# Kernel tuning notes

Hardware: AMD Instinct MI355X
Metric: run time of the kernel (lower is better)

The kernel has to match this reference:

```python
import jax, jax.numpy as jnp
import numpy as np

N_NODES = 50000
EMBED_DIM = 512
N_EDGES = 150000


def _edge_scores(node_embeddings, edges):
    # edges: [2, E] int; dot product of endpoint embeddings -> [E]
    src = node_embeddings[edges[0]]  # [E, D]
    dst = node_embeddings[edges[1]]  # [E, D]
    return jnp.sum(src * dst, axis=1)


def setup_inputs() -> dict:
    key = jax.random.key(0)
    k1, k2, k3 = jax.random.split(key, 3)
    node_embeddings = jax.random.normal(k1, (N_NODES, EMBED_DIM), dtype=jnp.float32)
    edge_index = jax.random.randint(k2, (2, N_EDGES), 0, N_NODES, dtype=jnp.int64)
    # negative edges: uniform random node pairs (matches the original sampler's
    # fallback distribution; precomputed so the reference is deterministic/jittable)
    neg_edges = jax.random.randint(k3, (2, N_EDGES), 0, N_NODES, dtype=jnp.int64)
    return {
        "node_embeddings": node_embeddings,
        "edge_index": edge_index,
        "neg_edges": neg_edges,
        "num_nodes": N_NODES,
    }


def reference(node_embeddings, edge_index, neg_edges, num_nodes):
    pos_scores = _edge_scores(node_embeddings, edge_index)  # [E]
    neg_scores = _edge_scores(node_embeddings, neg_edges)   # [E]
    all_scores = jnp.concatenate([pos_scores, neg_scores])
    all_labels = jnp.concatenate([
        jnp.ones_like(pos_scores),
        jnp.zeros_like(neg_scores),
    ])
    # BCE with logits: log(1 + exp(s)) - s*y, numerically stable via logaddexp
    per_elem = jnp.logaddexp(jnp.float32(0.0), all_scores) - all_scores * all_labels
    return jnp.mean(per_elem)
```

## Files before the change

### kernel.cpp

```cpp
#include <hip/hip_runtime.h>
#include <math.h>

#define N_EDGES   150000
#define TOTAL     300000
#define EMBED_DIM 512
#define N_NODES   50000
#define TABLE_ELEMS (N_NODES * EMBED_DIM)
#define TABLE_BYTES_F8 ((size_t)TABLE_ELEMS)
#define BLOCK_THREADS 256
#define CONV_BLOCKS 2048

#define GROUPS16   (TOTAL / 16)
#define POS_G16    (N_EDGES / 16)

#define NCHUNK       8
#define CHUNK_BYTES  64
#define SLICE_BYTES  ((size_t)N_NODES * CHUNK_BYTES)
#define PARTIAL_BYTES ((size_t)NCHUNK * TOTAL * 4)
#define WS_ACC_OFF   (TABLE_BYTES_F8 + PARTIAL_BYTES)
#define WS_NEEDED    (WS_ACC_OFF + 64)

#define SCORE_BLOCKS 2048
#define BLOCKS_PER_CHUNK (SCORE_BLOCKS / NCHUNK)
#define WAVES_PER_CHUNK  (BLOCKS_PER_CHUNK * 4)
#define RED_BLOCKS ((TOTAL + BLOCK_THREADS - 1) / BLOCK_THREADS)

typedef float floatx4 __attribute__((ext_vector_type(4)));
typedef unsigned long long ull;
typedef ull ull2 __attribute__((ext_vector_type(2)));

__global__ __launch_bounds__(BLOCK_THREADS) void convert_fp8_chunked(
    const float4* __restrict__ in,
    int*          __restrict__ out,
    float*        __restrict__ acc,
    unsigned int* __restrict__ cnt)
{
    if (blockIdx.x == 0 && threadIdx.x == 0) { *acc = 0.0f; *cnt = 0u; }
    const int stride = gridDim.x * blockDim.x;
    for (int i = blockIdx.x * blockDim.x + threadIdx.x;
         i < TABLE_ELEMS / 4; i += stride) {
        float4 v = in[i];
        int r = 0;
        r = __builtin_amdgcn_cvt_pk_fp8_f32(v.x, v.y, r, false);
        r = __builtin_amdgcn_cvt_pk_fp8_f32(v.z, v.w, r, true);
        const int node  = i >> 7;
        const int dim4  = i & 127;
        const int chunk = dim4 >> 4;
        const int w4    = dim4 & 15;
        out[(size_t)chunk * (N_NODES * 16) + (size_t)node * 16 + w4] = r;
    }
}

__global__ __launch_bounds__(BLOCK_THREADS, 8) void edge_score_chunked(
    const unsigned char* __restrict__ emb8,
    const int*           __restrict__ pos_edges,
    const int*           __restrict__ neg_edges,
    float*               __restrict__ partial)
{
    const int wave  = threadIdx.x >> 6;
    const int lane  = threadIdx.x & 63;
    const int chunk = blockIdx.x & 7;
    const int w     = (blockIdx.x >> 3) * 4 + wave;

    const int i    = lane & 15;
    const int quad = lane >> 4;
    const bool is_diag = ((i >> 2) == quad);
    const int  dreg    = i & 3;

    const unsigned char* __restrict__ slice = emb8 + (size_t)chunk * SLICE_BYTES;
    float* __restrict__ pout = partial + (size_t)chunk * TOTAL;

    for (int g = w; g < GROUPS16; g += WAVES_PER_CHUNK) {
        const bool is_pos = (g < POS_G16);
        const int* __restrict__ edges = is_pos ? pos_edges : neg_edges;
        const int  e0a = 16 * g - (is_pos ? 0 : N_EDGES);

        const int sidx = __builtin_nontemporal_load(edges + e0a + i);
        const int tidx = __builtin_nontemporal_load(edges + N_EDGES + e0a + i);

        const ull2 a = *(const ull2*)(slice + (size_t)(unsigned)sidx * CHUNK_BYTES + quad * 16);
        const ull2 b = *(const ull2*)(slice + (size_t)(unsigned)tidx * CHUNK_BYTES + quad * 16);

        floatx4 C = {0, 0, 0, 0};
        C = __builtin_amdgcn_mfma_f32_16x16x32_fp8_fp8((long)a[0], (long)b[0], C, 0, 0, 0);
        C = __builtin_amdgcn_mfma_f32_16x16x32_fp8_fp8((long)a[1], (long)b[1], C, 0, 0, 0);

        const float s = (dreg == 0) ? C[0] : (dreg == 1) ? C[1] : (dreg == 2) ? C[2] : C[3];
        if (is_diag)
            __builtin_nontemporal_store(s, pout + 16 * g + i);
    }
}

__global__ __launch_bounds__(BLOCK_THREADS) void reduce_bce_finalize(
    const float*  __restrict__ partial,
    float*        __restrict__ acc,
    unsigned int* __restrict__ cnt,
    float*        __restrict__ out)
{
    const int e = blockIdx.x * BLOCK_THREADS + threadIdx.x;
    float term = 0.0f;
    if (e < TOTAL) {
        float s = 0.0f;
        #pragma unroll
        for (int c = 0; c < NCHUNK; c++)
            s += partial[(size_t)c * TOTAL + e];
        const float sp = fmaxf(s, 0.0f) + log1pf(expf(-fabsf(s)));
        term = sp - (e < N_EDGES ? s : 0.0f);
    }
    #pragma unroll
    for (int off = 32; off > 0; off >>= 1)
        term += __shfl_down(term, off, 64);
    __shared__ float ls[4];
    if ((threadIdx.x & 63) == 0) ls[threadIdx.x >> 6] = term;
    __syncthreads();
    if (threadIdx.x == 0) {
        atomicAdd(acc, ls[0] + ls[1] + ls[2] + ls[3]);
        __threadfence();
        const unsigned prev = atomicAdd(cnt, 1u);
        if (prev == (unsigned)(gridDim.x - 1)) {
            __threadfence();
            const float tot = atomicAdd(acc, 0.0f);
            out[0] = tot * (1.0f / (float)TOTAL);
        }
    }
}

__global__ __launch_bounds__(BLOCK_THREADS) void convert_fp8(
    const float4* __restrict__ in,
    int*          __restrict__ out,
    float*        __restrict__ acc)
{
    if (blockIdx.x == 0 && threadIdx.x == 0) *acc = 0.0f;
    const int stride = gridDim.x * blockDim.x;
    for (int i = blockIdx.x * blockDim.x + threadIdx.x;
         i < TABLE_ELEMS / 4; i += stride) {
        float4 v = in[i];
        int r = 0;
        r = __builtin_amdgcn_cvt_pk_fp8_f32(v.x, v.y, r, false);
        r = __builtin_amdgcn_cvt_pk_fp8_f32(v.z, v.w, r, true);
        out[i] = r;
    }
}

#define EDGE_BLOCKS ((GROUPS16 + 3) / 4)
__global__ __launch_bounds__(BLOCK_THREADS, 4) void edge_loss_fp8(
    const unsigned char* __restrict__ emb8,
    const int*           __restrict__ pos_edges,
    const int*           __restrict__ neg_edges,
    float*               __restrict__ acc)
{
    const int wave = threadIdx.x >> 6;
    const int lane = threadIdx.x & 63;
    const int g    = blockIdx.x * 4 + wave;
    const int i    = lane & 15;
    const int quad = lane >> 4;
    const bool is_diag = ((i >> 2) == quad);
    const int  dreg    = i & 3;
    float contrib = 0.0f;
    if (g < GROUPS16) {
        const bool is_pos = (g < POS_G16);
        const int* __restrict__ edges = is_pos ? pos_edges : neg_edges;
        const int  e0 = 16 * g - (is_pos ? 0 : N_EDGES);
        const int sidx = edges[e0 + i];
        const int tidx = edges[N_EDGES + e0 + i];
        const ull2* rA = (const ull2*)(emb8 + (size_t)sidx * EMBED_DIM + quad * 16);
        const ull2* rB = (const ull2*)(emb8 + (size_t)tidx * EMBED_DIM + quad * 16);
        ull2 a[8], b[8];
        #pragma unroll
        for (int c = 0; c < 8; c++) { a[c] = rA[c * 4]; b[c] = rB[c * 4]; }
#if __has_builtin(__builtin_amdgcn_sched_barrier)
        __builtin_amdgcn_sched_barrier(0);
#endif
        floatx4 C0 = {0,0,0,0}, C1 = {0,0,0,0}, C2 = {0,0,0,0}, C3 = {0,0,0,0};
        #pragma unroll
        for (int c = 0; c < 2; c++) {
            #pragma unroll
            for (int h = 0; h < 2; h++) {
                C0 = __builtin_amdgcn_mfma_f32_16x16x32_fp8_fp8((long)a[c][h],     (long)b[c][h],     C0, 0, 0, 0);
                C1 = __builtin_amdgcn_mfma_f32_16x16x32_fp8_fp8((long)a[2 + c][h], (long)b[2 + c][h], C1, 0, 0, 0);
                C2 = __builtin_amdgcn_mfma_f32_16x16x32_fp8_fp8((long)a[4 + c][h], (long)b[4 + c][h], C2, 0, 0, 0);
                C3 = __builtin_amdgcn_mfma_f32_16x16x32_fp8_fp8((long)a[6 + c][h], (long)b[6 + c][h], C3, 0, 0, 0);
            }
        }
        floatx4 C = (C0 + C1) + (C2 + C3);
        float s = (dreg == 0) ? C[0] : (dreg == 1) ? C[1] : (dreg == 2) ? C[2] : C[3];
        float sp = fmaxf(s, 0.0f) + log1pf(expf(-fabsf(s)));
        contrib = is_diag ? (sp - (is_pos ? s : 0.0f)) : 0.0f;
    }
    #pragma unroll
    for (int off = 32; off > 0; off >>= 1)
        contrib += __shfl_down(contrib, off, 64);
    __shared__ float ls[4];
    if (lane == 0) ls[wave] = contrib;
    __syncthreads();
    if (threadIdx.x == 0)
        atomicAdd(acc, ls[0] + ls[1] + ls[2] + ls[3]);
}

#define N_PAIRS   (TOTAL / 2)
#define POS_PAIRS (N_EDGES / 2)
#define FB_WAVES  (CONV_BLOCKS * 4)
__global__ __launch_bounds__(BLOCK_THREADS, 8) void edge_loss_f32(
    const float* __restrict__ emb,
    const int*   __restrict__ pos_edges,
    const int*   __restrict__ neg_edges,
    float*       __restrict__ acc)
{
    const int wave  = threadIdx.x >> 6;
    const int lane  = threadIdx.x & 63;
    const int gwave = blockIdx.x * 4 + wave;
    float lsum = 0.0f;
    for (int g = gwave; g < N_PAIRS; g += FB_WAVES) {
        const bool is_pos = (g < POS_PAIRS);
        const int* __restrict__ edges = is_pos ? pos_edges : neg_edges;
        const int  e0 = 2 * g - (is_pos ? 0 : N_EDGES);
        const int s0 = edges[e0],     t0 = edges[N_EDGES + e0];
        const int s1 = edges[e0 + 1], t1 = edges[N_EDGES + e0 + 1];
        const float4* rS0 = (const float4*)(emb + (size_t)s0 * EMBED_DIM) + lane;
        const float4* rT0 = (const float4*)(emb + (size_t)t0 * EMBED_DIM) + lane;
        const float4* rS1 = (const float4*)(emb + (size_t)s1 * EMBED_DIM) + lane;
        const float4* rT1 = (const float4*)(emb + (size_t)t1 * EMBED_DIM) + lane;
        float4 a0 = rS0[0], a1 = rS0[64];
        float4 b0 = rT0[0], b1 = rT0[64];
        float4 c0 = rS1[0], c1 = rS1[64];
        float4 d0 = rT1[0], d1 = rT1[64];
        float p0 = fmaf(a0.x, b0.x, fmaf(a0.y, b0.y, fmaf(a0.z, b0.z, a0.w * b0.w)));
        float p1 = fmaf(a1.x, b1.x, fmaf(a1.y, b1.y, fmaf(a1.z, b1.z, a1.w * b1.w)));
        float q0 = fmaf(c0.x, d0.x, fmaf(c0.y, d0.y, fmaf(c0.z, d0.z, c0.w * d0.w)));
        float q1 = fmaf(c1.x, d1.x, fmaf(c1.y, d1.y, fmaf(c1.z, d1.z, c1.w * d1.w)));
        float p = p0 + p1, q = q0 + q1;
        #pragma unroll
        for (int off = 32; off > 0; off >>= 1) {
            p += __shfl_down(p, off, 64);
            q += __shfl_down(q, off, 64);
        }
        const float sp_p = fmaxf(p, 0.0f) + log1pf(expf(-fabsf(p)));
        const float sp_q = fmaxf(q, 0.0f) + log1pf(expf(-fabsf(q)));
        lsum += (lane == 0) ? (sp_p + sp_q - (is_pos ? (p + q) : 0.0f)) : 0.0f;
    }
    __shared__ float ls[4];
    if (lane == 0) ls[wave] = lsum;
    __syncthreads();
    if (threadIdx.x == 0)
        atomicAdd(acc, ls[0] + ls[1] + ls[2] + ls[3]);
}

__global__ void finalize_kernel(const float* __restrict__ acc, float* __restrict__ out)
{
    if (threadIdx.x == 0)
        out[0] = acc[0] * (1.0f / (float)TOTAL);
}

extern "C" void kernel_launch(void* const* d_in, const int* in_sizes, int n_in,
                              void* d_out, int out_size, void* d_ws, size_t ws_size,
                              hipStream_t stream) {
    const float* emb = (const float*)d_in[0];
    const int*   pos = (const int*)d_in[1];
    const int*   neg = (const int*)d_in[2];
    float* out = (float*)d_out;

    if (ws_size >= WS_NEEDED) {
        unsigned char* emb8    = (unsigned char*)d_ws;
        float*         partial = (float*)((char*)d_ws + TABLE_BYTES_F8);
        float*         acc     = (float*)((char*)d_ws + WS_ACC_OFF);
        unsigned int*  cnt     = (unsigned int*)((char*)d_ws + WS_ACC_OFF + 4);
        convert_fp8_chunked<<<CONV_BLOCKS, BLOCK_THREADS, 0, stream>>>(
            (const float4*)emb, (int*)d_ws, acc, cnt);
        edge_score_chunked<<<SCORE_BLOCKS, BLOCK_THREADS, 0, stream>>>(
            emb8, pos, neg, partial);
        reduce_bce_finalize<<<RED_BLOCKS, BLOCK_THREADS, 0, stream>>>(
            partial, acc, cnt, out);
    } else if (ws_size >= TABLE_BYTES_F8 + 64) {
        unsigned char* emb8 = (unsigned char*)d_ws;
        float*         acc  = (float*)((char*)d_ws + TABLE_BYTES_F8);
        convert_fp8<<<CONV_BLOCKS, BLOCK_THREADS, 0, stream>>>(
            (const float4*)emb, (int*)d_ws, acc);
        edge_loss_fp8<<<EDGE_BLOCKS, BLOCK_THREADS, 0, stream>>>(emb8, pos, neg, acc);
        finalize_kernel<<<1, 64, 0, stream>>>(acc, out);
    } else {
        float* acc = (float*)d_ws;
        (void)hipMemsetAsync(acc, 0, sizeof(float), stream);
        edge_loss_f32<<<CONV_BLOCKS, BLOCK_THREADS, 0, stream>>>(emb, pos, neg, acc);
        finalize_kernel<<<1, 64, 0, stream>>>(acc, out);
    }
}
```

Measured before the change: 243.7 us.

## Bind embedding chunks to XCC IDs with atomic span work-stealing

The score kernel now reads the hardware XCC ID and uses it to pick which 64-byte embedding chunk slice to process. Each slice (3.2 MB) should then stay resident in that XCD's L2 rather than relying on the block-to-XCD mapping. Work is handed out dynamically through a per-chunk atomic counter in spans of 24 groups, and each wave processes two groups per iteration for more memory-level parallelism. The convert kernel is reordered so its writes are contiguous and its reads strided, and it zeroes the claim counters. A risk is that an unbalanced number of blocks per XCC leaves chunks processed unevenly, and the atomic-plus-syncthreads loop adds overhead.

```diff
diff --git a/kernel.cpp b/kernel.cpp
--- a/kernel.cpp
+++ b/kernel.cpp
@@ -21,8 +21,9 @@
 #define WS_NEEDED    (WS_ACC_OFF + 64)
 
 #define SCORE_BLOCKS 2048
-#define BLOCKS_PER_CHUNK (SCORE_BLOCKS / NCHUNK)
-#define WAVES_PER_CHUNK  (BLOCKS_PER_CHUNK * 4)
+#define SPAN_GROUPS  24
+#define G_PER_WAVE   6
+#define NSPANS       ((GROUPS16 + SPAN_GROUPS - 1) / SPAN_GROUPS)
 #define RED_BLOCKS ((TOTAL + BLOCK_THREADS - 1) / BLOCK_THREADS)
 
 typedef float floatx4 __attribute__((ext_vector_type(4)));
@@ -33,21 +34,25 @@
     const float4* __restrict__ in,
     int*          __restrict__ out,
     float*        __restrict__ acc,
-    unsigned int* __restrict__ cnt)
-{
-    if (blockIdx.x == 0 && threadIdx.x == 0) { *acc = 0.0f; *cnt = 0u; }
+    unsigned int* __restrict__ cnt,
+    int*          __restrict__ claim)
+{
+    if (blockIdx.x == 0 && threadIdx.x < 16) {
+        if (threadIdx.x == 0) { *acc = 0.0f; *cnt = 0u; }
+        if (threadIdx.x < NCHUNK) claim[threadIdx.x] = 0;
+    }
     const int stride = gridDim.x * blockDim.x;
-    for (int i = blockIdx.x * blockDim.x + threadIdx.x;
-         i < TABLE_ELEMS / 4; i += stride) {
-        float4 v = in[i];
+    for (int o = blockIdx.x * blockDim.x + threadIdx.x;
+         o < TABLE_ELEMS / 4; o += stride) {
+        const int chunk = o / (N_NODES * 16);
+        const int rem   = o - chunk * (N_NODES * 16);
+        const int node  = rem >> 4;
+        const int w4    = rem & 15;
+        float4 v = in[node * 128 + chunk * 16 + w4];
         int r = 0;
         r = __builtin_amdgcn_cvt_pk_fp8_f32(v.x, v.y, r, false);
         r = __builtin_amdgcn_cvt_pk_fp8_f32(v.z, v.w, r, true);
-        const int node  = i >> 7;
-        const int dim4  = i & 127;
-        const int chunk = dim4 >> 4;
-        const int w4    = dim4 & 15;
-        out[(size_t)chunk * (N_NODES * 16) + (size_t)node * 16 + w4] = r;
+        out[o] = r;
     }
 }
 
@@ -55,13 +60,15 @@
     const unsigned char* __restrict__ emb8,
     const int*           __restrict__ pos_edges,
     const int*           __restrict__ neg_edges,
-    float*               __restrict__ partial)
-{
-    const int wave  = threadIdx.x >> 6;
-    const int lane  = threadIdx.x & 63;
-    const int chunk = blockIdx.x & 7;
-    const int w     = (blockIdx.x >> 3) * 4 + wave;
-
+    float*               __restrict__ partial,
+    int*                 __restrict__ claim)
+{
+    unsigned int xcc;
+    asm volatile("s_getreg_b32 %0, hwreg(HW_REG_XCC_ID)" : "=s"(xcc));
+    const int chunk = (int)(xcc & 7u);
+
+    const int wave = threadIdx.x >> 6;
+    const int lane = threadIdx.x & 63;
     const int i    = lane & 15;
     const int quad = lane >> 4;
     const bool is_diag = ((i >> 2) == quad);
@@ -70,24 +77,51 @@
     const unsigned char* __restrict__ slice = emb8 + (size_t)chunk * SLICE_BYTES;
     float* __restrict__ pout = partial + (size_t)chunk * TOTAL;
 
-    for (int g = w; g < GROUPS16; g += WAVES_PER_CHUNK) {
-        const bool is_pos = (g < POS_G16);
-        const int* __restrict__ edges = is_pos ? pos_edges : neg_edges;
-        const int  e0a = 16 * g - (is_pos ? 0 : N_EDGES);
-
-        const int sidx = __builtin_nontemporal_load(edges + e0a + i);
-        const int tidx = __builtin_nontemporal_load(edges + N_EDGES + e0a + i);
-
-        const ull2 a = *(const ull2*)(slice + (size_t)(unsigned)sidx * CHUNK_BYTES + quad * 16);
-        const ull2 b = *(const ull2*)(slice + (size_t)(unsigned)tidx * CHUNK_BYTES + quad * 16);
-
-        floatx4 C = {0, 0, 0, 0};
-        C = __builtin_amdgcn_mfma_f32_16x16x32_fp8_fp8((long)a[0], (long)b[0], C, 0, 0, 0);
-        C = __builtin_amdgcn_mfma_f32_16x16x32_fp8_fp8((long)a[1], (long)b[1], C, 0, 0, 0);
-
-        const float s = (dreg == 0) ? C[0] : (dreg == 1) ? C[1] : (dreg == 2) ? C[2] : C[3];
-        if (is_diag)
-            __builtin_nontemporal_store(s, pout + 16 * g + i);
+    __shared__ int sspan;
+    for (;;) {
+        if (threadIdx.x == 0) sspan = atomicAdd(claim + chunk, 1);
+        __syncthreads();
+        const int span = sspan;
+        __syncthreads();
+        if (span >= NSPANS) break;
+
+        const int gb = span * SPAN_GROUPS + wave * G_PER_WAVE;
+        #pragma unroll
+        for (int u = 0; u < G_PER_WAVE / 2; u++) {
+            int g0 = gb + 2 * u;
+            if (g0 > GROUPS16 - 1) g0 = GROUPS16 - 1;
+            int g1 = g0 + 1;
+            if (g1 > GROUPS16 - 1) g1 = GROUPS16 - 1;
+
+            const bool p0 = (g0 < POS_G16), p1 = (g1 < POS_G16);
+            const int* __restrict__ ed0 = p0 ? pos_edges : neg_edges;
+            const int* __restrict__ ed1 = p1 ? pos_edges : neg_edges;
+            const int e00 = 16 * g0 - (p0 ? 0 : N_EDGES);
+            const int e01 = 16 * g1 - (p1 ? 0 : N_EDGES);
+
+            const int s0 = __builtin_nontemporal_load(ed0 + e00 + i);
+            const int t0 = __builtin_nontemporal_load(ed0 + N_EDGES + e00 + i);
+            const int s1 = __builtin_nontemporal_load(ed1 + e01 + i);
+            const int t1 = __builtin_nontemporal_load(ed1 + N_EDGES + e01 + i);
+
+            const ull2 a0 = *(const ull2*)(slice + (size_t)(unsigned)s0 * CHUNK_BYTES + quad * 16);
+            const ull2 b0 = *(const ull2*)(slice + (size_t)(unsigned)t0 * CHUNK_BYTES + quad * 16);
+            const ull2 a1 = *(const ull2*)(slice + (size_t)(unsigned)s1 * CHUNK_BYTES + quad * 16);
+            const ull2 b1 = *(const ull2*)(slice + (size_t)(unsigned)t1 * CHUNK_BYTES + quad * 16);
+
+            floatx4 C0 = {0, 0, 0, 0}, C1 = {0, 0, 0, 0};
+            C0 = __builtin_amdgcn_mfma_f32_16x16x32_fp8_fp8((long)a0[0], (long)b0[0], C0, 0, 0, 0);
+            C0 = __builtin_amdgcn_mfma_f32_16x16x32_fp8_fp8((long)a0[1], (long)b0[1], C0, 0, 0, 0);
+            C1 = __builtin_amdgcn_mfma_f32_16x16x32_fp8_fp8((long)a1[0], (long)b1[0], C1, 0, 0, 0);
+            C1 = __builtin_amdgcn_mfma_f32_16x16x32_fp8_fp8((long)a1[1], (long)b1[1], C1, 0, 0, 0);
+
+            const float sc0 = (dreg == 0) ? C0[0] : (dreg == 1) ? C0[1] : (dreg == 2) ? C0[2] : C0[3];
+            const float sc1 = (dreg == 0) ? C1[0] : (dreg == 1) ? C1[1] : (dreg == 2) ? C1[2] : C1[3];
+            if (is_diag) {
+                __builtin_nontemporal_store(sc0, pout + 16 * g0 + i);
+                __builtin_nontemporal_store(sc1, pout + 16 * g1 + i);
+            }
+        }
     }
 }
 
@@ -264,10 +298,11 @@
         float*         partial = (float*)((char*)d_ws + TABLE_BYTES_F8);
         float*         acc     = (float*)((char*)d_ws + WS_ACC_OFF);
         unsigned int*  cnt     = (unsigned int*)((char*)d_ws + WS_ACC_OFF + 4);
+        int*           claim   = (int*)((char*)d_ws + WS_ACC_OFF + 8);
         convert_fp8_chunked<<<CONV_BLOCKS, BLOCK_THREADS, 0, stream>>>(
-            (const float4*)emb, (int*)d_ws, acc, cnt);
+            (const float4*)emb, (int*)d_ws, acc, cnt, claim);
         edge_score_chunked<<<SCORE_BLOCKS, BLOCK_THREADS, 0, stream>>>(
-            emb8, pos, neg, partial);
+            emb8, pos, neg, partial, claim);
         reduce_bce_finalize<<<RED_BLOCKS, BLOCK_THREADS, 0, stream>>>(
             partial, acc, cnt, out);
     } else if (ws_size >= TABLE_BYTES_F8 + 64) {
```

After: 296.7 us. 1.22x slower.
